# Kernel tuning notes

Hardware: AMD Instinct MI355X
Metric: run time of the kernel (lower is better)

Reference implementation:

```python
import jax, jax.numpy as jnp
import numpy as np

B, T, C, H = 2, 2048, 1024, 16
D = C // H  # head_dim = 64

def setup_inputs() -> dict:
    key = jax.random.key(0)
    k1, k2, k3, k4, k5 = jax.random.split(key, 5)
    x = jax.random.normal(k1, (B, T, C), dtype=jnp.float32)
    # RoPE tables (realistic frequencies)
    inv_freq = 1.0 / (10000.0 ** (jnp.arange(0, D // 2, dtype=jnp.float32) / (D // 2)))
    pos = jnp.arange(T, dtype=jnp.float32)
    ang = pos[:, None] * inv_freq[None, :]          # (T, D/2)
    cos, sin = jnp.cos(ang), jnp.sin(ang)
    # causal mask (True = keep)
    mask = jnp.tril(jnp.ones((T, T), dtype=bool))
    W_qkv = jax.random.normal(k2, (3 * C, C), dtype=jnp.float32) * (1.0 / np.sqrt(C))
    W_out = jax.random.normal(k3, (C, C), dtype=jnp.float32) * (1.0 / np.sqrt(C))
    return {"x": x, "cos": cos, "sin": sin, "mask": mask, "W_qkv": W_qkv, "W_out": W_out}

def apply_rope(x, cos, sin):
    # x: (B, H, T, D); cos/sin: (T, D/2)
    d = x.shape[-1] // 2
    x1, x2 = x[..., :d], x[..., d:]
    c = cos[None, None, :x.shape[2], :]
    s = sin[None, None, :x.shape[2], :]
    return jnp.concatenate([x1 * c - x2 * s, x2 * c + x1 * s], axis=-1)

def reference(x, cos, sin, mask, W_qkv, W_out):
    b, t, c = x.shape
    qkv = (x @ W_qkv.T).reshape(b, t, 3, H, D)
    q, k, v = qkv[:, :, 0], qkv[:, :, 1], qkv[:, :, 2]   # (b, t, H, D)
    q = q.transpose(0, 2, 1, 3)
    k = k.transpose(0, 2, 1, 3)
    v = v.transpose(0, 2, 1, 3)                           # (b, H, t, D)
    q = apply_rope(q, cos, sin)
    k = apply_rope(k, cos, sin)
    attn = jnp.einsum('bhqd,bhkd->bhqk', q, k) / jnp.sqrt(jnp.asarray(D, x.dtype))
    attn = jnp.where(mask[None, None, :, :], attn, -jnp.inf)
    attn = jax.nn.softmax(attn, axis=-1)
    out = jnp.einsum('bhqk,bhkd->bhqd', attn, v)          # (b, H, t, D)
    out = out.transpose(0, 2, 1, 3).reshape(b, t, c)
    return out @ W_out.T
```

## Files before the change

kernel.cpp:

```cpp
#include <hip/hip_runtime.h>
#include <stdint.h>

typedef __bf16 bf16;
typedef __bf16 bf16x4 __attribute__((ext_vector_type(4)));
typedef __bf16 bf16x8 __attribute__((ext_vector_type(8)));
typedef float f32x4 __attribute__((ext_vector_type(4)));

#define TSEQ 2048
#define NHEAD 16
#define HDIM 64
#define CDIM 1024

#if __has_builtin(__builtin_amdgcn_exp2f)
#define EXP2(x) __builtin_amdgcn_exp2f(x)
#else
#define EXP2(x) exp2f(x)
#endif

__device__ __forceinline__ bf16x8 load8(const float* p) {
  const float4 a = *(const float4*)p;
  const float4 b = *(const float4*)(p + 4);
  bf16x8 r;
  r[0] = (bf16)a.x; r[1] = (bf16)a.y; r[2] = (bf16)a.z; r[3] = (bf16)a.w;
  r[4] = (bf16)b.x; r[5] = (bf16)b.y; r[6] = (bf16)b.z; r[7] = (bf16)b.w;
  return r;
}
__device__ __forceinline__ bf16x8 load8(const bf16* p) { return *(const bf16x8*)p; }

__global__ __launch_bounds__(256) void gemm_qkv_rope(const float* __restrict__ A,
                                                     const float* __restrict__ B,
                                                     const float* __restrict__ cosb,
                                                     const float* __restrict__ sinb,
                                                     bf16* __restrict__ Qb,
                                                     bf16* __restrict__ Kb,
                                                     bf16* __restrict__ Vraw) {
  constexpr int K = 1024;
  constexpr int LDT = 40;
  __shared__ bf16 As[128 * LDT];
  __shared__ bf16 Bs[128 * LDT];
  const int t = threadIdx.x;
  const int w = t >> 6, l = t & 63, g = l >> 4, ln = l & 15;
  const int wm = (w >> 1) * 64, wn = (w & 1) * 64;
  const int m0 = blockIdx.x * 128, n0 = blockIdx.y * 128;
  const int r0 = t >> 2, kc0 = (t & 3) * 8;

  f32x4 acc[4][4] = {};

  for (int k0 = 0; k0 < K; k0 += 32) {
    bf16x8 a0 = load8(A + (size_t)(m0 + r0) * K + k0 + kc0);
    bf16x8 a1 = load8(A + (size_t)(m0 + r0 + 64) * K + k0 + kc0);
    bf16x8 b0 = load8(B + (size_t)(n0 + r0) * K + k0 + kc0);
    bf16x8 b1 = load8(B + (size_t)(n0 + r0 + 64) * K + k0 + kc0);
    __syncthreads();
    *(bf16x8*)&As[r0 * LDT + kc0] = a0;
    *(bf16x8*)&As[(r0 + 64) * LDT + kc0] = a1;
    *(bf16x8*)&Bs[r0 * LDT + kc0] = b0;
    *(bf16x8*)&Bs[(r0 + 64) * LDT + kc0] = b1;
    __syncthreads();
    bf16x8 af[4], bfr[4];
#pragma unroll
    for (int i = 0; i < 4; i++) {
      af[i] = *(const bf16x8*)&As[(wm + i * 16 + ln) * LDT + g * 8];
      bfr[i] = *(const bf16x8*)&Bs[(wn + i * 16 + ln) * LDT + g * 8];
    }
#pragma unroll
    for (int i = 0; i < 4; i++)
#pragma unroll
      for (int j = 0; j < 4; j++)
        acc[i][j] = __builtin_amdgcn_mfma_f32_16x16x32_bf16(af[i], bfr[j], acc[i][j], 0, 0, 0);
  }

  const int part = n0 >> 10;
  if (part < 2) {
    bf16* dst = part ? Kb : Qb;
    const float qs = part ? 1.0f : 0.18033688011112042f;
#pragma unroll
    for (int i = 0; i < 4; i++)
#pragma unroll
      for (int j = 0; j < 2; j++) {
        int nl = (n0 & 1023) + wn + j * 16 + ln;
        int h = nl >> 6, d = nl & 31;
#pragma unroll
        for (int r = 0; r < 4; r++) {
          int row = m0 + wm + i * 16 + g * 4 + r;
          int tok = row & (TSEQ - 1), bb = row >> 11;
          float c = cosb[tok * 32 + d], s = sinb[tok * 32 + d];
          float a1 = acc[i][j][r], a2 = acc[i][j + 2][r];
          size_t ob = ((size_t)(bb * NHEAD + h) * TSEQ + tok) * HDIM + d;
          dst[ob] = (bf16)((a1 * c - a2 * s) * qs);
          dst[ob + 32] = (bf16)((a2 * c + a1 * s) * qs);
        }
      }
  } else {
#pragma unroll
    for (int i = 0; i < 4; i++)
#pragma unroll
      for (int j = 0; j < 4; j++) {
        int nl = (n0 & 1023) + wn + j * 16 + ln;
#pragma unroll
        for (int r = 0; r < 4; r++) {
          int row = m0 + wm + i * 16 + g * 4 + r;
          Vraw[(size_t)row * 1024 + nl] = (bf16)acc[i][j][r];
        }
      }
  }
}

template <typename TA, typename TB, typename TC>
__global__ __launch_bounds__(256) void gemm_nt(const TA* __restrict__ A,
                                               const TB* __restrict__ B,
                                               TC* __restrict__ C,
                                               int M, int N, int K) {
  constexpr int LDT = 40;
  __shared__ bf16 As[128 * LDT];
  __shared__ bf16 Bs[128 * LDT];
  const int t = threadIdx.x;
  const int w = t >> 6, l = t & 63, g = l >> 4, ln = l & 15;
  const int wm = (w >> 1) * 64, wn = (w & 1) * 64;
  const int m0 = blockIdx.x * 128, n0 = blockIdx.y * 128;
  const int r0 = t >> 2, kc0 = (t & 3) * 8;

  f32x4 acc[4][4] = {};

  for (int k0 = 0; k0 < K; k0 += 32) {
    bf16x8 a0 = load8(A + (size_t)(m0 + r0) * K + k0 + kc0);
    bf16x8 a1 = load8(A + (size_t)(m0 + r0 + 64) * K + k0 + kc0);
    bf16x8 b0 = load8(B + (size_t)(n0 + r0) * K + k0 + kc0);
    bf16x8 b1 = load8(B + (size_t)(n0 + r0 + 64) * K + k0 + kc0);
    __syncthreads();
    *(bf16x8*)&As[r0 * LDT + kc0] = a0;
    *(bf16x8*)&As[(r0 + 64) * LDT + kc0] = a1;
    *(bf16x8*)&Bs[r0 * LDT + kc0] = b0;
    *(bf16x8*)&Bs[(r0 + 64) * LDT + kc0] = b1;
    __syncthreads();
    bf16x8 af[4], bfr[4];
#pragma unroll
    for (int i = 0; i < 4; i++) {
      af[i] = *(const bf16x8*)&As[(wm + i * 16 + ln) * LDT + g * 8];
      bfr[i] = *(const bf16x8*)&Bs[(wn + i * 16 + ln) * LDT + g * 8];
    }
#pragma unroll
    for (int i = 0; i < 4; i++)
#pragma unroll
      for (int j = 0; j < 4; j++)
        acc[i][j] = __builtin_amdgcn_mfma_f32_16x16x32_bf16(af[i], bfr[j], acc[i][j], 0, 0, 0);
  }
#pragma unroll
  for (int i = 0; i < 4; i++)
#pragma unroll
    for (int j = 0; j < 4; j++) {
      int row = m0 + wm + i * 16 + g * 4;
      int col = n0 + wn + j * 16 + ln;
#pragma unroll
      for (int r = 0; r < 4; r++)
        C[(size_t)(row + r) * N + col] = (TC)acc[i][j][r];
    }
}

__global__ __launch_bounds__(256) void transpose_v(const bf16* __restrict__ Vraw,
                                                   bf16* __restrict__ Vt) {
  __shared__ bf16 Vs[64 * 72];
  const int t = threadIdx.x;
  const int tt = blockIdx.x;
  const int bh = blockIdx.y;
  const int b = bh >> 4, h = bh & (NHEAD - 1);
  for (int c = t; c < 512; c += 256) {
    int row = c >> 3, ch = c & 7;
    bf16x8 v = *(const bf16x8*)(Vraw + (size_t)(b * TSEQ + tt * 64 + row) * 1024 +
                                h * HDIM + ch * 8);
    *(bf16x8*)&Vs[row * 72 + ch * 8] = v;
  }
  __syncthreads();
  for (int c = t; c < 512; c += 256) {
    int d = c >> 3, ch = c & 7;
    bf16x8 o;
#pragma unroll
    for (int j = 0; j < 8; j++) o[j] = Vs[(ch * 8 + j) * 72 + d];
    *(bf16x8*)(Vt + ((size_t)(bh * HDIM + d)) * TSEQ + tt * 64 + ch * 8) = o;
  }
}

__global__ __launch_bounds__(512) void attn_fwd(const bf16* __restrict__ Q,
                                                const bf16* __restrict__ K,
                                                const bf16* __restrict__ Vt,
                                                bf16* __restrict__ ctx) {
  __shared__ bf16 Ks[2][64 * 72];
  __shared__ bf16 VTs[2][64 * 72];
  __shared__ bf16 Ps[8][16 * 72];
  __shared__ float Mrg[4][64][16];
  __shared__ float lred[4][16];
  __shared__ float linv[4][16];

  const int t = threadIdx.x;
  const int gp = t >> 8;
  const int tl = t & 255;
  const int w = t >> 6;
  const int w2 = w & 3;
  const int l = t & 63, g = l >> 4, ln = l & 15;
  const int pr = blockIdx.x, bh = blockIdx.y;
  const size_t base = (size_t)bh * TSEQ * HDIM;

  const int r0 = tl >> 3, r1 = (tl + 256) >> 3, ch0 = (tl & 7) * 8;
  bf16x8 kr0, kr1, vr0, vr1;

  for (int half = 0; half < 2; half++) {
    const int qb = half ? (31 - pr) : pr;
    const int q0 = qb * 64;
    const int q_global = q0 + w2 * 16 + ln;
    bf16x8 bq[2];
    bq[0] = *(const bf16x8*)(Q + base + (size_t)q_global * HDIM + g * 8);
    bq[1] = *(const bf16x8*)(Q + base + (size_t)q_global * HDIM + 32 + g * 8);
    f32x4 acc[4] = {};
    float l_run = 0.f;
    const int nit = (qb >> 1) + 1;

    if (gp <= qb) {
      kr0 = *(const bf16x8*)(K + base + (size_t)(gp * 64 + r0) * HDIM + ch0);
      kr1 = *(const bf16x8*)(K + base + (size_t)(gp * 64 + r1) * HDIM + ch0);
      vr0 = *(const bf16x8*)(Vt + base + (size_t)r0 * TSEQ + gp * 64 + ch0);
      vr1 = *(const bf16x8*)(Vt + base + (size_t)r1 * TSEQ + gp * 64 + ch0);
    }

    for (int i = 0; i < nit; i++) {
      const int kt = 2 * i + gp;
      const bool active = (kt <= qb);
      __syncthreads();
      if (active) {
        *(bf16x8*)&Ks[gp][r0 * 72 + ch0] = kr0;
        *(bf16x8*)&Ks[gp][r1 * 72 + ch0] = kr1;
        *(bf16x8*)&VTs[gp][r0 * 72 + ch0] = vr0;
        *(bf16x8*)&VTs[gp][r1 * 72 + ch0] = vr1;
      }
      __syncthreads();
      const int ktn = kt + 2;
      if (ktn <= qb) {
        kr0 = *(const bf16x8*)(K + base + (size_t)(ktn * 64 + r0) * HDIM + ch0);
        kr1 = *(const bf16x8*)(K + base + (size_t)(ktn * 64 + r1) * HDIM + ch0);
        vr0 = *(const bf16x8*)(Vt + base + (size_t)r0 * TSEQ + ktn * 64 + ch0);
        vr1 = *(const bf16x8*)(Vt + base + (size_t)r1 * TSEQ + ktn * 64 + ch0);
      }
      if (active) {
        f32x4 st[4] = {};
#pragma unroll
        for (int step = 0; step < 2; step++)
#pragma unroll
          for (int mt = 0; mt < 4; mt++) {
            bf16x8 ak = *(const bf16x8*)&Ks[gp][(mt * 16 + ln) * 72 + step * 32 + g * 8];
            st[mt] = __builtin_amdgcn_mfma_f32_16x16x32_bf16(ak, bq[step], st[mt], 0, 0, 0);
          }
        float vals[16];
        if (kt == qb) {
#pragma unroll
          for (int mt = 0; mt < 4; mt++)
#pragma unroll
            for (int r = 0; r < 4; r++) {
              int kg = kt * 64 + mt * 16 + g * 4 + r;
              vals[mt * 4 + r] = (kg <= q_global) ? fminf(st[mt][r], 60.f) : -INFINITY;
            }
        } else {
#pragma unroll
          for (int mt = 0; mt < 4; mt++)
#pragma unroll
            for (int r = 0; r < 4; r++) vals[mt * 4 + r] = fminf(st[mt][r], 60.f);
        }
        float psum = 0.f;
#pragma unroll
        for (int i2 = 0; i2 < 16; i2++) {
          float p = EXP2(vals[i2]);
          vals[i2] = p;
          psum += p;
        }
        psum += __shfl_xor(psum, 16);
        psum += __shfl_xor(psum, 32);
        l_run += psum;
#pragma unroll
        for (int mt = 0; mt < 4; mt++) {
          bf16x4 pk;
#pragma unroll
          for (int r = 0; r < 4; r++) pk[r] = (bf16)vals[mt * 4 + r];
          *(bf16x4*)&Ps[w][ln * 72 + mt * 16 + g * 4] = pk;
        }
#pragma unroll
        for (int step = 0; step < 2; step++) {
          bf16x8 ap = *(const bf16x8*)&Ps[w][ln * 72 + step * 32 + g * 8];
#pragma unroll
          for (int nt = 0; nt < 4; nt++) {
            bf16x8 bv = *(const bf16x8*)&VTs[gp][(nt * 16 + ln) * 72 + step * 32 + g * 8];
            acc[nt] = __builtin_amdgcn_mfma_f32_16x16x32_bf16(ap, bv, acc[nt], 0, 0, 0);
          }
        }
      }
    }
    __syncthreads();
    if (gp == 1) {
#pragma unroll
      for (int nt = 0; nt < 4; nt++) *(f32x4*)&Mrg[w2][l][nt * 4] = acc[nt];
      if (l < 16) lred[w2][ln] = l_run;
    }
    __syncthreads();
    if (gp == 0) {
#pragma unroll
      for (int nt = 0; nt < 4; nt++) acc[nt] += *(const f32x4*)&Mrg[w2][l][nt * 4];
      float ltot = l_run + lred[w2][ln];
      if (l < 16) linv[w2][ln] = 1.0f / ltot;
      float lrow[4];
#pragma unroll
      for (int r = 0; r < 4; r++) lrow[r] = linv[w2][g * 4 + r];
      const int b = bh >> 4, h = bh & (NHEAD - 1);
#pragma unroll
      for (int nt = 0; nt < 4; nt++)
#pragma unroll
        for (int r = 0; r < 4; r++) {
          int q = q0 + w2 * 16 + g * 4 + r;
          ctx[(size_t)(b * TSEQ + q) * CDIM + h * HDIM + nt * 16 + ln] =
              (bf16)(acc[nt][r] * lrow[r]);
        }
    }
  }
}

extern "C" void kernel_launch(void* const* d_in, const int* in_sizes, int n_in,
                              void* d_out, int out_size, void* d_ws, size_t ws_size,
                              hipStream_t stream) {
  const float* x = (const float*)d_in[0];
  const float* cosb = (const float*)d_in[1];
  const float* sinb = (const float*)d_in[2];
  const float* Wqkv = (const float*)d_in[4];
  const float* Wout = (const float*)d_in[5];
  float* out = (float*)d_out;

  char* ws = (char*)d_ws;
  bf16* Qb = (bf16*)ws;
  bf16* Kb = (bf16*)(ws + 8388608);
  bf16* Vt = (bf16*)(ws + 16777216);
  bf16* Vraw = (bf16*)(ws + 25165824);
  bf16* ctx = (bf16*)(ws + 33554432);

  gemm_qkv_rope<<<dim3(32, 24), 256, 0, stream>>>(x, Wqkv, cosb, sinb, Qb, Kb, Vraw);
  transpose_v<<<dim3(32, 32), 256, 0, stream>>>(Vraw, Vt);
  attn_fwd<<<dim3(16, 2 * NHEAD), 512, 0, stream>>>(Qb, Kb, Vt, ctx);
  gemm_nt<bf16, float, float><<<dim3(32, 8), 256, 0, stream>>>(ctx, Wout, out, 4096, 1024, 1024);
}
```

Baseline: 215.3 us.

## Pre-cast GEMM inputs to bf16 and stage tiles via direct global-to-LDS loads

Adds separate cast kernels that convert x, W_qkv and W_out from fp32 to bf16 once, so both GEMMs read bf16 operands. The GEMM tile loads now use global_load_lds to copy straight into shared memory, with unpadded 32-wide rows, instead of going through registers and ds_write. This halves GEMM operand bandwidth and frees VGPRs, at the cost of extra cast launches and fp32 round-trip traffic. The removed row padding may bring back LDS bank conflicts. Workspace buffers are reshuffled and aliased (ctx shares with x_bf, Wout_bf with Wqkv_bf).

```diff
diff --git a/kernel.cpp b/kernel.cpp
--- a/kernel.cpp
+++ b/kernel.cpp
@@ -10,6 +10,9 @@
 #define NHEAD 16
 #define HDIM 64
 #define CDIM 1024
+
+#define AS1(p) ((const __attribute__((address_space(1))) void*)(p))
+#define AS3(p) ((__attribute__((address_space(3))) void*)(p))
 
 #if __has_builtin(__builtin_amdgcn_exp2f)
 #define EXP2(x) __builtin_amdgcn_exp2f(x)
@@ -17,27 +20,50 @@
 #define EXP2(x) exp2f(x)
 #endif
 
-__device__ __forceinline__ bf16x8 load8(const float* p) {
-  const float4 a = *(const float4*)p;
-  const float4 b = *(const float4*)(p + 4);
+__global__ __launch_bounds__(256) void cast_bf16(const float* __restrict__ in,
+                                                 bf16* __restrict__ out, int n) {
+  int i = (blockIdx.x * 256 + threadIdx.x) * 8;
+  if (i >= n) return;
+  float4 a = *(const float4*)(in + i);
+  float4 b = *(const float4*)(in + i + 4);
   bf16x8 r;
   r[0] = (bf16)a.x; r[1] = (bf16)a.y; r[2] = (bf16)a.z; r[3] = (bf16)a.w;
   r[4] = (bf16)b.x; r[5] = (bf16)b.y; r[6] = (bf16)b.z; r[7] = (bf16)b.w;
-  return r;
-}
-__device__ __forceinline__ bf16x8 load8(const bf16* p) { return *(const bf16x8*)p; }
-
-__global__ __launch_bounds__(256) void gemm_qkv_rope(const float* __restrict__ A,
-                                                     const float* __restrict__ B,
+  *(bf16x8*)(out + i) = r;
+}
+
+__global__ __launch_bounds__(256) void cast2_bf16(const float* __restrict__ in1, int n1,
+                                                  const float* __restrict__ in2, int n2,
+                                                  bf16* __restrict__ out1,
+                                                  bf16* __restrict__ out2) {
+  int i = (blockIdx.x * 256 + threadIdx.x) * 8;
+  const float* src;
+  bf16* dst;
+  if (i < n1) {
+    src = in1 + i; dst = out1 + i;
+  } else if (i < n1 + n2) {
+    src = in2 + (i - n1); dst = out2 + (i - n1);
+  } else {
+    return;
+  }
+  float4 a = *(const float4*)src;
+  float4 b = *(const float4*)(src + 4);
+  bf16x8 r;
+  r[0] = (bf16)a.x; r[1] = (bf16)a.y; r[2] = (bf16)a.z; r[3] = (bf16)a.w;
+  r[4] = (bf16)b.x; r[5] = (bf16)b.y; r[6] = (bf16)b.z; r[7] = (bf16)b.w;
+  *(bf16x8*)dst = r;
+}
+
+__global__ __launch_bounds__(256) void gemm_qkv_rope(const bf16* __restrict__ A,
+                                                     const bf16* __restrict__ B,
                                                      const float* __restrict__ cosb,
                                                      const float* __restrict__ sinb,
                                                      bf16* __restrict__ Qb,
                                                      bf16* __restrict__ Kb,
                                                      bf16* __restrict__ Vraw) {
   constexpr int K = 1024;
-  constexpr int LDT = 40;
-  __shared__ bf16 As[128 * LDT];
-  __shared__ bf16 Bs[128 * LDT];
+  __shared__ bf16 As[128 * 32];
+  __shared__ bf16 Bs[128 * 32];
   const int t = threadIdx.x;
   const int w = t >> 6, l = t & 63, g = l >> 4, ln = l & 15;
   const int wm = (w >> 1) * 64, wn = (w & 1) * 64;
@@ -47,21 +73,21 @@
   f32x4 acc[4][4] = {};
 
   for (int k0 = 0; k0 < K; k0 += 32) {
-    bf16x8 a0 = load8(A + (size_t)(m0 + r0) * K + k0 + kc0);
-    bf16x8 a1 = load8(A + (size_t)(m0 + r0 + 64) * K + k0 + kc0);
-    bf16x8 b0 = load8(B + (size_t)(n0 + r0) * K + k0 + kc0);
-    bf16x8 b1 = load8(B + (size_t)(n0 + r0 + 64) * K + k0 + kc0);
-    __syncthreads();
-    *(bf16x8*)&As[r0 * LDT + kc0] = a0;
-    *(bf16x8*)&As[(r0 + 64) * LDT + kc0] = a1;
-    *(bf16x8*)&Bs[r0 * LDT + kc0] = b0;
-    *(bf16x8*)&Bs[(r0 + 64) * LDT + kc0] = b1;
+    __syncthreads();
+    __builtin_amdgcn_global_load_lds(AS1(A + (size_t)(m0 + r0) * K + k0 + kc0),
+                                     AS3(&As[t * 8]), 16, 0, 0);
+    __builtin_amdgcn_global_load_lds(AS1(A + (size_t)(m0 + r0 + 64) * K + k0 + kc0),
+                                     AS3(&As[(t + 256) * 8]), 16, 0, 0);
+    __builtin_amdgcn_global_load_lds(AS1(B + (size_t)(n0 + r0) * K + k0 + kc0),
+                                     AS3(&Bs[t * 8]), 16, 0, 0);
+    __builtin_amdgcn_global_load_lds(AS1(B + (size_t)(n0 + r0 + 64) * K + k0 + kc0),
+                                     AS3(&Bs[(t + 256) * 8]), 16, 0, 0);
     __syncthreads();
     bf16x8 af[4], bfr[4];
 #pragma unroll
     for (int i = 0; i < 4; i++) {
-      af[i] = *(const bf16x8*)&As[(wm + i * 16 + ln) * LDT + g * 8];
-      bfr[i] = *(const bf16x8*)&Bs[(wn + i * 16 + ln) * LDT + g * 8];
+      af[i] = *(const bf16x8*)&As[(wm + i * 16 + ln) * 32 + g * 8];
+      bfr[i] = *(const bf16x8*)&Bs[(wn + i * 16 + ln) * 32 + g * 8];
     }
 #pragma unroll
     for (int i = 0; i < 4; i++)
@@ -106,14 +132,13 @@
   }
 }
 
-template <typename TA, typename TB, typename TC>
-__global__ __launch_bounds__(256) void gemm_nt(const TA* __restrict__ A,
-                                               const TB* __restrict__ B,
+template <typename TC>
+__global__ __launch_bounds__(256) void gemm_nt(const bf16* __restrict__ A,
+                                               const bf16* __restrict__ B,
                                                TC* __restrict__ C,
                                                int M, int N, int K) {
-  constexpr int LDT = 40;
-  __shared__ bf16 As[128 * LDT];
-  __shared__ bf16 Bs[128 * LDT];
+  __shared__ bf16 As[128 * 32];
+  __shared__ bf16 Bs[128 * 32];
   const int t = threadIdx.x;
   const int w = t >> 6, l = t & 63, g = l >> 4, ln = l & 15;
   const int wm = (w >> 1) * 64, wn = (w & 1) * 64;
@@ -123,21 +148,21 @@
   f32x4 acc[4][4] = {};
 
   for (int k0 = 0; k0 < K; k0 += 32) {
-    bf16x8 a0 = load8(A + (size_t)(m0 + r0) * K + k0 + kc0);
-    bf16x8 a1 = load8(A + (size_t)(m0 + r0 + 64) * K + k0 + kc0);
-    bf16x8 b0 = load8(B + (size_t)(n0 + r0) * K + k0 + kc0);
-    bf16x8 b1 = load8(B + (size_t)(n0 + r0 + 64) * K + k0 + kc0);
-    __syncthreads();
-    *(bf16x8*)&As[r0 * LDT + kc0] = a0;
-    *(bf16x8*)&As[(r0 + 64) * LDT + kc0] = a1;
-    *(bf16x8*)&Bs[r0 * LDT + kc0] = b0;
-    *(bf16x8*)&Bs[(r0 + 64) * LDT + kc0] = b1;
+    __syncthreads();
+    __builtin_amdgcn_global_load_lds(AS1(A + (size_t)(m0 + r0) * K + k0 + kc0),
+                                     AS3(&As[t * 8]), 16, 0, 0);
+    __builtin_amdgcn_global_load_lds(AS1(A + (size_t)(m0 + r0 + 64) * K + k0 + kc0),
+                                     AS3(&As[(t + 256) * 8]), 16, 0, 0);
+    __builtin_amdgcn_global_load_lds(AS1(B + (size_t)(n0 + r0) * K + k0 + kc0),
+                                     AS3(&Bs[t * 8]), 16, 0, 0);
+    __builtin_amdgcn_global_load_lds(AS1(B + (size_t)(n0 + r0 + 64) * K + k0 + kc0),
+                                     AS3(&Bs[(t + 256) * 8]), 16, 0, 0);
     __syncthreads();
     bf16x8 af[4], bfr[4];
 #pragma unroll
     for (int i = 0; i < 4; i++) {
-      af[i] = *(const bf16x8*)&As[(wm + i * 16 + ln) * LDT + g * 8];
-      bfr[i] = *(const bf16x8*)&Bs[(wn + i * 16 + ln) * LDT + g * 8];
+      af[i] = *(const bf16x8*)&As[(wm + i * 16 + ln) * 32 + g * 8];
+      bfr[i] = *(const bf16x8*)&Bs[(wn + i * 16 + ln) * 32 + g * 8];
     }
 #pragma unroll
     for (int i = 0; i < 4; i++)
@@ -330,14 +355,20 @@
   float* out = (float*)d_out;
 
   char* ws = (char*)d_ws;
-  bf16* Qb = (bf16*)ws;
-  bf16* Kb = (bf16*)(ws + 8388608);
-  bf16* Vt = (bf16*)(ws + 16777216);
-  bf16* Vraw = (bf16*)(ws + 25165824);
-  bf16* ctx = (bf16*)(ws + 33554432);
-
-  gemm_qkv_rope<<<dim3(32, 24), 256, 0, stream>>>(x, Wqkv, cosb, sinb, Qb, Kb, Vraw);
+  bf16* x_bf = (bf16*)ws;
+  bf16* ctx = (bf16*)ws;
+  bf16* Wqkv_bf = (bf16*)(ws + 8388608);
+  bf16* Wout_bf = (bf16*)(ws + 8388608);
+  bf16* Qb = (bf16*)(ws + 14680064);
+  bf16* Kb = (bf16*)(ws + 23068672);
+  bf16* Vraw = (bf16*)(ws + 31457280);
+  bf16* Vt = (bf16*)(ws + 39845888);
+
+  cast2_bf16<<<(4194304 + 3145728) / 8 / 256, 256, 0, stream>>>(
+      x, 4194304, Wqkv, 3145728, x_bf, Wqkv_bf);
+  gemm_qkv_rope<<<dim3(32, 24), 256, 0, stream>>>(x_bf, Wqkv_bf, cosb, sinb, Qb, Kb, Vraw);
+  cast_bf16<<<1048576 / 8 / 256, 256, 0, stream>>>(Wout, Wout_bf, 1048576);
   transpose_v<<<dim3(32, 32), 256, 0, stream>>>(Vraw, Vt);
   attn_fwd<<<dim3(16, 2 * NHEAD), 512, 0, stream>>>(Qb, Kb, Vt, ctx);
-  gemm_nt<bf16, float, float><<<dim3(32, 8), 256, 0, stream>>>(ctx, Wout, out, 4096, 1024, 1024);
-}
+  gemm_nt<float><<<dim3(32, 8), 256, 0, stream>>>(ctx, Wout_bf, out, 4096, 1024, 1024);
+}
```

Result: faster. 205.5 us (-4.5%).
